# Kernel optimization log

Measured on AMD Instinct MI355X. Metric: run time of the kernel, lower is better.

## Reference

```python
import jax, jax.numpy as jnp
import numpy as np

N_HEAD = 16


def setup_inputs() -> dict:
    key = jax.random.key(0)
    k1, k2, k3 = jax.random.split(key, 3)
    B, T, C = 4, 2048, 1024
    x = jax.random.normal(k1, (B, T, C), dtype=jnp.float32)
    Wqkv = jax.random.normal(k2, (C, 3 * C), dtype=jnp.float32) * 0.02
    Wproj = jax.random.normal(k3, (C, C), dtype=jnp.float32) * 0.02
    return {"x": x, "Wqkv": Wqkv, "Wproj": Wproj}


def reference(x, Wqkv, Wproj):
    B, T, C = x.shape
    nh = N_HEAD
    hd = C // nh
    qkv = x @ Wqkv                                  # (B, T, 3C)
    q, k, v = jnp.split(qkv, 3, axis=-1)
    # (B, T, C) -> (B, nh, T, hd)
    q = q.reshape(B, T, nh, hd).transpose(0, 2, 1, 3)
    k = k.reshape(B, T, nh, hd).transpose(0, 2, 1, 3)
    v = v.reshape(B, T, nh, hd).transpose(0, 2, 1, 3)
    # scaled dot-product attention with causal mask (past_kv=None => T_all == T)
    att = jnp.einsum("bhtd,bhsd->bhts", q, k) / jnp.sqrt(jnp.float32(hd))
    causal = jnp.tril(jnp.ones((T, T), dtype=bool))  # (T, T)
    att = jnp.where(causal[None, None, :, :], att, jnp.float32(-jnp.inf))
    att = jax.nn.softmax(att, axis=-1)              # (B, nh, T, T)
    y = jnp.einsum("bhts,bhsd->bhtd", att, v)       # (B, nh, T, hd)
    y = y.transpose(0, 2, 1, 3).reshape(B, T, C)
    y = y @ Wproj                                   # (B, T, C)
    # present_kv (detached in original)
    return y, jax.lax.stop_gradient(k), jax.lax.stop_gradient(v)
```

## Files before the change

kernel.cpp:

```cpp
#include <hip/hip_runtime.h>
#include <hip/hip_bf16.h>


typedef __bf16 bf16;
typedef __attribute__((ext_vector_type(8))) __bf16 bf16x8;
typedef __attribute__((ext_vector_type(4))) __bf16 bf16x4;
typedef __attribute__((ext_vector_type(4))) float f32x4;

#define AS_G __attribute__((address_space(1)))
#define AS_L __attribute__((address_space(3)))

#define QSCALE 0.1803368801111204f

__device__ __forceinline__ void gld_lds16(const bf16* g, bf16* l) {
  __builtin_amdgcn_global_load_lds((const AS_G void*)g, (AS_L void*)l, 16, 0, 0);
}

__global__ __launch_bounds__(256) void k_cast(const float* __restrict__ in,
                                              bf16* __restrict__ out, int n) {
  int i = (blockIdx.x * 256 + threadIdx.x) * 8;
  if (i >= n) return;
  float4 a = *(const float4*)(in + i);
  float4 b = *(const float4*)(in + i + 4);
  bf16x8 o;
  o[0] = (bf16)a.x; o[1] = (bf16)a.y; o[2] = (bf16)a.z; o[3] = (bf16)a.w;
  o[4] = (bf16)b.x; o[5] = (bf16)b.y; o[6] = (bf16)b.z; o[7] = (bf16)b.w;
  *(bf16x8*)(out + i) = o;
}

__global__ __launch_bounds__(256) void k_transpose(const float* __restrict__ in,
                                                   bf16* __restrict__ out,
                                                   int K, int N) {
  __shared__ float tile[32][33];
  int bx = blockIdx.x * 32;
  int by = blockIdx.y * 32;
  int tx = threadIdx.x, ty = threadIdx.y;
#pragma unroll
  for (int i = 0; i < 4; ++i)
    tile[ty + i * 8][tx] = in[(size_t)(by + ty + i * 8) * N + bx + tx];
  __syncthreads();
#pragma unroll
  for (int i = 0; i < 4; ++i)
    out[(size_t)(bx + ty + i * 8) * K + by + tx] = (bf16)tile[tx][ty + i * 8];
}

__device__ __forceinline__ void gemm_main_256x128(const bf16* __restrict__ A,
                                                  const bf16* __restrict__ Bt,
                                                  int m0, int n0,
                                                  bf16* As, bf16* Bs,
                                                  f32x4 acc[4][4]) {
  const int tid = threadIdx.x;
  const int w = tid >> 6, lane = tid & 63, lo = lane & 15, hi = lane >> 4;
  const int wm = w >> 1, wn = w & 1;
  const int urow = tid >> 3;
  const int gsw = (tid & 7) ^ (urow & 7);
  const bf16* ga = A + (size_t)(m0 + urow) * 1024 + gsw * 8;
  const bf16* gb = Bt + (size_t)(n0 + urow) * 1024 + gsw * 8;
  const int p0 = hi ^ (lo & 7);
  const int aRow = wm * 64 + lo;
  const int bRow = wn * 64 + lo;

#define STAGE_A2(t, bufi, s0) do {                                                              \
    gld_lds16(ga + (size_t)(s0) * 65536 + (t) * 64,                                             \
              As + (bufi) * 16384 + (s0) * 4096 + w * 512);                                     \
    gld_lds16(ga + (size_t)((s0) + 1) * 65536 + (t) * 64,                                       \
              As + (bufi) * 16384 + ((s0) + 1) * 4096 + w * 512);                               \
  } while (0)
#define STAGE_B2(t, bufi) do {                                                                  \
    gld_lds16(gb + (t) * 64, Bs + (bufi) * 8192 + w * 512);                                     \
    gld_lds16(gb + 65536 + (t) * 64, Bs + (bufi) * 8192 + 4096 + w * 512);                      \
  } while (0)

  STAGE_A2(0, 0, 0); STAGE_A2(0, 0, 2); STAGE_B2(0, 0);
  STAGE_A2(1, 1, 0); STAGE_A2(1, 1, 2); STAGE_B2(1, 1);

  bf16x8 a[2][2], b[4][2];
  int buf = 0, sbuf = 2;
#pragma unroll 1
  for (int t = 0; t < 16; ++t) {
    if (t < 15) asm volatile("s_waitcnt vmcnt(6)" ::: "memory");
    else        asm volatile("s_waitcnt vmcnt(0)" ::: "memory");
    __builtin_amdgcn_s_barrier();
    const bf16* Ab = As + buf * 16384;
    const bf16* Bb = Bs + buf * 8192;

#pragma unroll
    for (int mi = 0; mi < 2; ++mi) {
      const bf16* r = Ab + (aRow + mi * 16) * 64;
      a[mi][0] = *(const bf16x8*)(r + p0 * 8);
      a[mi][1] = *(const bf16x8*)(r + (p0 ^ 4) * 8);
    }
#pragma unroll
    for (int ni = 0; ni < 2; ++ni) {
      const bf16* r = Bb + (bRow + ni * 16) * 64;
      b[ni][0] = *(const bf16x8*)(r + p0 * 8);
      b[ni][1] = *(const bf16x8*)(r + (p0 ^ 4) * 8);
    }
    if (t < 14) STAGE_A2(t + 2, sbuf, 0);
    __builtin_amdgcn_s_barrier();
    __builtin_amdgcn_s_setprio(1);
#pragma unroll
    for (int ks = 0; ks < 2; ++ks)
#pragma unroll
      for (int mi = 0; mi < 2; ++mi)
#pragma unroll
        for (int ni = 0; ni < 2; ++ni)
          acc[mi][ni] = __builtin_amdgcn_mfma_f32_16x16x32_bf16(a[mi][ks], b[ni][ks], acc[mi][ni], 0, 0, 0);
    __builtin_amdgcn_s_setprio(0);
    __builtin_amdgcn_s_barrier();

#pragma unroll
    for (int ni = 0; ni < 2; ++ni) {
      const bf16* r = Bb + (bRow + (ni + 2) * 16) * 64;
      b[ni + 2][0] = *(const bf16x8*)(r + p0 * 8);
      b[ni + 2][1] = *(const bf16x8*)(r + (p0 ^ 4) * 8);
    }
    if (t < 14) STAGE_A2(t + 2, sbuf, 2);
    __builtin_amdgcn_s_barrier();
    __builtin_amdgcn_s_setprio(1);
#pragma unroll
    for (int ks = 0; ks < 2; ++ks)
#pragma unroll
      for (int mi = 0; mi < 2; ++mi)
#pragma unroll
        for (int ni = 0; ni < 2; ++ni)
          acc[mi][ni + 2] = __builtin_amdgcn_mfma_f32_16x16x32_bf16(a[mi][ks], b[ni + 2][ks], acc[mi][ni + 2], 0, 0, 0);
    __builtin_amdgcn_s_setprio(0);
    __builtin_amdgcn_s_barrier();

#pragma unroll
    for (int mi = 0; mi < 2; ++mi) {
      const bf16* r = Ab + (aRow + (mi + 2) * 16) * 64;
      a[mi][0] = *(const bf16x8*)(r + p0 * 8);
      a[mi][1] = *(const bf16x8*)(r + (p0 ^ 4) * 8);
    }
    if (t < 14) STAGE_B2(t + 2, sbuf);
    __builtin_amdgcn_s_barrier();
    __builtin_amdgcn_s_setprio(1);
#pragma unroll
    for (int ks = 0; ks < 2; ++ks)
#pragma unroll
      for (int mi = 0; mi < 2; ++mi)
#pragma unroll
        for (int ni = 0; ni < 2; ++ni)
          acc[mi + 2][ni + 2] = __builtin_amdgcn_mfma_f32_16x16x32_bf16(a[mi][ks], b[ni + 2][ks], acc[mi + 2][ni + 2], 0, 0, 0);
    __builtin_amdgcn_s_setprio(0);
    __builtin_amdgcn_s_barrier();

    __builtin_amdgcn_s_setprio(1);
#pragma unroll
    for (int ks = 0; ks < 2; ++ks)
#pragma unroll
      for (int mi = 0; mi < 2; ++mi)
#pragma unroll
        for (int ni = 0; ni < 2; ++ni)
          acc[mi + 2][ni] = __builtin_amdgcn_mfma_f32_16x16x32_bf16(a[mi][ks], b[ni][ks], acc[mi + 2][ni], 0, 0, 0);
    __builtin_amdgcn_s_setprio(0);

    buf = (buf == 2) ? 0 : buf + 1;
    sbuf = (sbuf == 2) ? 0 : sbuf + 1;
  }
#undef STAGE_A2
#undef STAGE_B2
}

__global__ __launch_bounds__(512, 2) void k_gemm_qkv(const bf16* __restrict__ x,
                                                     const bf16* __restrict__ WqkvT,
                                                     bf16* __restrict__ qb, bf16* __restrict__ kb,
                                                     bf16* __restrict__ vtb,
                                                     float* __restrict__ outk, float* __restrict__ outv) {
  __shared__ bf16 As[49152], Bs[24576];
  int id = blockIdx.x;
  int swz = (id & 7) * 96 + (id >> 3);
  int by = swz / 24, bx = swz - by * 24;
  int m0 = by * 256, n0 = bx * 128;
  f32x4 acc[4][4] = {};
  gemm_main_256x128(x, WqkvT, m0, n0, As, Bs, acc);
  const int tid = threadIdx.x;
  const int w = tid >> 6, lane = tid & 63, lo = lane & 15, hi = lane >> 4;
  const int wm = w >> 1, wn = w & 1;
#pragma unroll
  for (int mi = 0; mi < 4; ++mi) {
    int growbase = m0 + wm * 64 + mi * 16 + hi * 4;
    int bb = growbase >> 11, t0 = growbase & 2047;
#pragma unroll
    for (int ni = 0; ni < 4; ++ni) {
      int gcol = n0 + wn * 64 + ni * 16 + lo;
      int part = gcol >> 10;
      int cc = gcol & 1023, h = cc >> 6, d = cc & 63;
      size_t idx0 = ((size_t)(bb * 16 + h) * 2048 + t0) * 64 + d;
      if (part == 0) {
#pragma unroll
        for (int r = 0; r < 4; ++r) qb[idx0 + (size_t)r * 64] = (bf16)(acc[mi][ni][r] * QSCALE);
      } else if (part == 1) {
#pragma unroll
        for (int r = 0; r < 4; ++r) {
          float val = acc[mi][ni][r];
          kb[idx0 + (size_t)r * 64] = (bf16)val;
          outk[idx0 + (size_t)r * 64] = val;
        }
      } else {
        bf16x4 pk;
#pragma unroll
        for (int r = 0; r < 4; ++r) {
          float val = acc[mi][ni][r];
          outv[idx0 + (size_t)r * 64] = val;
          pk[r] = (bf16)val;
        }
        *(bf16x4*)(vtb + ((size_t)(bb * 16 + h) * 64 + d) * 2048 + t0) = pk;
      }
    }
  }
}

__global__ __launch_bounds__(512, 2) void k_gemm_proj(const bf16* __restrict__ yb,
                                                      const bf16* __restrict__ WprojT,
                                                      float* __restrict__ out) {
  __shared__ bf16 As[49152], Bs[24576];
  int id = blockIdx.x;
  int swz = (id & 7) * 32 + (id >> 3);
  int by = swz >> 3, bx = swz & 7;
  int m0 = by * 256, n0 = bx * 128;
  f32x4 acc[4][4] = {};
  gemm_main_256x128(yb, WprojT, m0, n0, As, Bs, acc);
  const int tid = threadIdx.x;
  const int w = tid >> 6, lane = tid & 63, lo = lane & 15, hi = lane >> 4;
  const int wm = w >> 1, wn = w & 1;
#pragma unroll
  for (int mi = 0; mi < 4; ++mi)
#pragma unroll
    for (int ni = 0; ni < 4; ++ni)
#pragma unroll
      for (int r = 0; r < 4; ++r) {
        int grow = m0 + wm * 64 + mi * 16 + hi * 4 + r;
        int gcol = n0 + wn * 64 + ni * 16 + lo;
        out[(size_t)grow * 1024 + gcol] = acc[mi][ni][r];
      }
}

__device__ __forceinline__ void p_store(f32x4 sacc[4], bool mask,
                                        int w, int lo, int hi, bf16* psrow) {
  if (mask) {
#pragma unroll
    for (int nt = 0; nt < 4; ++nt)
#pragma unroll
      for (int r = 0; r < 4; ++r)
        if (nt * 16 + hi * 4 + r > w * 16 + lo) sacc[nt][r] = -1e30f;
  }
#pragma unroll
  for (int nt = 0; nt < 4; ++nt) {
    bf16x4 pk;
#pragma unroll
    for (int r = 0; r < 4; ++r) pk[r] = (bf16)exp2f(sacc[nt][r]);
    *(bf16x4*)(psrow + (w * 16 + lo) * 72 + nt * 16 + hi * 4) = pk;
  }
}

__device__ __forceinline__ void write_y(bf16* __restrict__ y, int b, int h, int qrow,
                                        int hi, const f32x4 o[4], float inv) {
  size_t base = ((size_t)b * 2048 + qrow) * 1024 + h * 64;
#pragma unroll
  for (int mt = 0; mt < 4; ++mt) {
    bf16x4 yk;
#pragma unroll
    for (int r = 0; r < 4; ++r) yk[r] = (bf16)(o[mt][r] * inv);
    *(bf16x4*)(y + base + mt * 16 + hi * 4) = yk;
  }
}

__global__ __launch_bounds__(256, 4) void k_flash(const bf16* __restrict__ q,
                                                  const bf16* __restrict__ k,
                                                  const bf16* __restrict__ vt,
                                                  bf16* __restrict__ y) {
  __shared__ bf16 Ks[64 * 64];
  __shared__ bf16 Vs[80 * 64];
  __shared__ bf16 Ps[128 * 72];
  const int bi = blockIdx.x;
  const int slot = bi >> 3;
  const int bh = (bi & 7) + 8 * (slot >> 4);
  const int j = slot & 15;
  const int jA = j, jB = 31 - j;
  const int tid = threadIdx.x, w = tid >> 6, lane = tid & 63, lo = lane & 15, hi = lane >> 4;
  const bf16* qp = q + (size_t)bh * 2048 * 64;
  const bf16* kp = k + (size_t)bh * 2048 * 64;
  const bf16* vtp = vt + (size_t)bh * 64 * 2048;

  {
    int rr = tid >> 4, c = (tid & 15) * 4;
    bf16x4 z;
    bf16 v1 = (rr == 0) ? (bf16)1.0f : (bf16)0.0f;
    z[0] = v1; z[1] = v1; z[2] = v1; z[3] = v1;
    *(bf16x4*)(Vs + (64 + rr) * 64 + c) = z;
  }

  bf16x8 qfA[2], qfB[2];
  {
    int qA = jA * 64 + w * 16 + lo;
    int qB = jB * 64 + w * 16 + lo;
    qfA[0] = *(const bf16x8*)(qp + (size_t)qA * 64 + hi * 8);
    qfA[1] = *(const bf16x8*)(qp + (size_t)qA * 64 + 32 + hi * 8);
    qfB[0] = *(const bf16x8*)(qp + (size_t)qB * 64 + hi * 8);
    qfB[1] = *(const bf16x8*)(qp + (size_t)qB * 64 + 32 + hi * 8);
  }
  f32x4 oA[4] = {}, oB[4] = {};
  f32x4 oLA = {}, oLB = {};

  for (int st = 0; st <= jB; ++st) {
    const int s0 = st * 64;
#pragma unroll
    for (int p = 0; p < 2; ++p) {
      int u = tid + 256 * p;
      int row = u >> 3, c = u & 7, g = c ^ (row & 7);
      gld_lds16(kp + (size_t)(s0 + row) * 64 + g * 8, Ks + p * 2048 + w * 512);
      gld_lds16(vtp + (size_t)row * 2048 + s0 + g * 8, Vs + p * 2048 + w * 512);
    }
    __syncthreads();

    bf16x8 kf[4][2];
#pragma unroll
    for (int nt = 0; nt < 4; ++nt)
#pragma unroll
      for (int ks = 0; ks < 2; ++ks)
        kf[nt][ks] = *(const bf16x8*)(Ks + (nt * 16 + lo) * 64 + ((ks * 4 + hi) ^ (lo & 7)) * 8);

    const bool actA = (st <= jA);
    if (actA) {
      f32x4 sacc[4] = {};
#pragma unroll
      for (int nt = 0; nt < 4; ++nt)
#pragma unroll
        for (int ks = 0; ks < 2; ++ks)
          sacc[nt] = __builtin_amdgcn_mfma_f32_16x16x32_bf16(kf[nt][ks], qfA[ks], sacc[nt], 0, 0, 0);
      p_store(sacc, st == jA, w, lo, hi, Ps);
    }
    {
      f32x4 sacc[4] = {};
#pragma unroll
      for (int nt = 0; nt < 4; ++nt)
#pragma unroll
        for (int ks = 0; ks < 2; ++ks)
          sacc[nt] = __builtin_amdgcn_mfma_f32_16x16x32_bf16(kf[nt][ks], qfB[ks], sacc[nt], 0, 0, 0);
      p_store(sacc, st == jB, w, lo, hi, Ps + 64 * 72);
    }
    __asm__ volatile("s_waitcnt lgkmcnt(0)" ::: "memory");

    bf16x8 pfA[2], pfB[2];
#pragma unroll
    for (int ks = 0; ks < 2; ++ks) {
      pfB[ks] = *(const bf16x8*)(Ps + (64 + w * 16 + lo) * 72 + ks * 32 + hi * 8);
      if (actA) pfA[ks] = *(const bf16x8*)(Ps + (w * 16 + lo) * 72 + ks * 32 + hi * 8);
    }
#pragma unroll
    for (int mt = 0; mt < 5; ++mt) {
#pragma unroll
      for (int ks = 0; ks < 2; ++ks) {
        int row = mt * 16 + lo;
        bf16x8 vf = *(const bf16x8*)(Vs + row * 64 + ((ks * 4 + hi) ^ (row & 7)) * 8);
        if (mt < 4) {
          oB[mt] = __builtin_amdgcn_mfma_f32_16x16x32_bf16(vf, pfB[ks], oB[mt], 0, 0, 0);
          if (actA) oA[mt] = __builtin_amdgcn_mfma_f32_16x16x32_bf16(vf, pfA[ks], oA[mt], 0, 0, 0);
        } else {
          oLB = __builtin_amdgcn_mfma_f32_16x16x32_bf16(vf, pfB[ks], oLB, 0, 0, 0);
          if (actA) oLA = __builtin_amdgcn_mfma_f32_16x16x32_bf16(vf, pfA[ks], oLA, 0, 0, 0);
        }
      }
    }
    __syncthreads();
  }

  const int b = bh >> 4, h = bh & 15;
  float lA = __shfl(oLA[0], lo, 64);
  float lB = __shfl(oLB[0], lo, 64);
  write_y(y, b, h, jA * 64 + w * 16 + lo, hi, oA, 1.0f / lA);
  write_y(y, b, h, jB * 64 + w * 16 + lo, hi, oB, 1.0f / lB);
}

extern "C" void kernel_launch(void* const* d_in, const int* in_sizes, int n_in,
                              void* d_out, int out_size, void* d_ws, size_t ws_size,
                              hipStream_t stream) {
  const float* x = (const float*)d_in[0];
  const float* Wqkv = (const float*)d_in[1];
  const float* Wproj = (const float*)d_in[2];
  float* out = (float*)d_out;

  const size_t YSZ = (size_t)8192 * 1024;
  char* ws = (char*)d_ws;
  bf16* xb = (bf16*)ws;      ws += (size_t)8192 * 1024 * 2;
  bf16* wqkvT = (bf16*)ws;   ws += (size_t)3072 * 1024 * 2;
  bf16* wprojT = (bf16*)ws;  ws += (size_t)1024 * 1024 * 2;
  bf16* qb = (bf16*)ws;      ws += (size_t)64 * 2048 * 64 * 2;
  bf16* kb = (bf16*)ws;      ws += (size_t)64 * 2048 * 64 * 2;
  bf16* vtb = (bf16*)ws;     ws += (size_t)64 * 2048 * 64 * 2;
  bf16* yb = (bf16*)ws;

  float* outy = out;
  float* outk = out + YSZ;
  float* outv = out + 2 * YSZ;

  k_cast<<<4096, 256, 0, stream>>>(x, xb, 8388608);
  dim3 tb(32, 8);
  k_transpose<<<dim3(96, 32), tb, 0, stream>>>(Wqkv, wqkvT, 1024, 3072);
  k_transpose<<<dim3(32, 32), tb, 0, stream>>>(Wproj, wprojT, 1024, 1024);
  k_gemm_qkv<<<768, 512, 0, stream>>>(xb, wqkvT, qb, kb, vtb, outk, outv);
  k_flash<<<1024, 256, 0, stream>>>(qb, kb, vtb, yb);
  k_gemm_proj<<<256, 512, 0, stream>>>(yb, wprojT, outy);
}
```

Measured before the change: 309.0 us.

## Double-buffer K/V in flash kernel and merge prep kernels into one launch

The flash attention kernel now double-buffers K and V tiles in LDS, prefetching the next tile while computing the current one, and waits on vmcnt before a barrier instead of using a synchronous load-then-sync loop. The ones-row used for the row-sum trick moves to its own LDS buffer, the P stride changes to 76 to reduce bank conflicts, raw exp2 is used, and s_setprio is raised around MFMA blocks. The cast and two transpose kernels are merged into a single launch to cut launch overhead. The extra LDS reduces the room for multiple blocks per CU, which may cost occupancy.

```diff
diff --git a/kernel.cpp b/kernel.cpp
--- a/kernel.cpp
+++ b/kernel.cpp
@@ -16,32 +16,34 @@
   __builtin_amdgcn_global_load_lds((const AS_G void*)g, (AS_L void*)l, 16, 0, 0);
 }
 
-__global__ __launch_bounds__(256) void k_cast(const float* __restrict__ in,
-                                              bf16* __restrict__ out, int n) {
-  int i = (blockIdx.x * 256 + threadIdx.x) * 8;
-  if (i >= n) return;
-  float4 a = *(const float4*)(in + i);
-  float4 b = *(const float4*)(in + i + 4);
-  bf16x8 o;
-  o[0] = (bf16)a.x; o[1] = (bf16)a.y; o[2] = (bf16)a.z; o[3] = (bf16)a.w;
-  o[4] = (bf16)b.x; o[5] = (bf16)b.y; o[6] = (bf16)b.z; o[7] = (bf16)b.w;
-  *(bf16x8*)(out + i) = o;
-}
-
-__global__ __launch_bounds__(256) void k_transpose(const float* __restrict__ in,
-                                                   bf16* __restrict__ out,
-                                                   int K, int N) {
+__global__ __launch_bounds__(256) void k_prep(const float* __restrict__ x, bf16* __restrict__ xb,
+                                              const float* __restrict__ Wqkv, bf16* __restrict__ wqkvT,
+                                              const float* __restrict__ Wproj, bf16* __restrict__ wprojT) {
   __shared__ float tile[32][33];
-  int bx = blockIdx.x * 32;
-  int by = blockIdx.y * 32;
-  int tx = threadIdx.x, ty = threadIdx.y;
+  const int bid = blockIdx.x, tid = threadIdx.x;
+  if (bid < 4096) {
+    int i = (bid * 256 + tid) * 8;
+    float4 a = *(const float4*)(x + i);
+    float4 b = *(const float4*)(x + i + 4);
+    bf16x8 o;
+    o[0] = (bf16)a.x; o[1] = (bf16)a.y; o[2] = (bf16)a.z; o[3] = (bf16)a.w;
+    o[4] = (bf16)b.x; o[5] = (bf16)b.y; o[6] = (bf16)b.z; o[7] = (bf16)b.w;
+    *(bf16x8*)(xb + i) = o;
+    return;
+  }
+  const float* in; bf16* out; int N, t;
+  if (bid < 7168) { t = bid - 4096; N = 3072; in = Wqkv; out = wqkvT; }
+  else            { t = bid - 7168; N = 1024; in = Wproj; out = wprojT; }
+  const int nbx = N >> 5;
+  const int bx = (t % nbx) * 32, by = (t / nbx) * 32;
+  const int tx = tid & 31, ty = tid >> 5;
 #pragma unroll
   for (int i = 0; i < 4; ++i)
     tile[ty + i * 8][tx] = in[(size_t)(by + ty + i * 8) * N + bx + tx];
   __syncthreads();
 #pragma unroll
   for (int i = 0; i < 4; ++i)
-    out[(size_t)(bx + ty + i * 8) * K + by + tx] = (bf16)tile[tx][ty + i * 8];
+    out[(size_t)(bx + ty + i * 8) * 1024 + by + tx] = (bf16)tile[tx][ty + i * 8];
 }
 
 __device__ __forceinline__ void gemm_main_256x128(const bf16* __restrict__ A,
@@ -238,6 +240,8 @@
       }
 }
 
+#define PSTR 76
+
 __device__ __forceinline__ void p_store(f32x4 sacc[4], bool mask,
                                         int w, int lo, int hi, bf16* psrow) {
   if (mask) {
@@ -251,8 +255,8 @@
   for (int nt = 0; nt < 4; ++nt) {
     bf16x4 pk;
 #pragma unroll
-    for (int r = 0; r < 4; ++r) pk[r] = (bf16)exp2f(sacc[nt][r]);
-    *(bf16x4*)(psrow + (w * 16 + lo) * 72 + nt * 16 + hi * 4) = pk;
+    for (int r = 0; r < 4; ++r) pk[r] = (bf16)__builtin_amdgcn_exp2f(sacc[nt][r]);
+    *(bf16x4*)(psrow + (w * 16 + lo) * PSTR + nt * 16 + hi * 4) = pk;
   }
 }
 
@@ -272,9 +276,10 @@
                                                   const bf16* __restrict__ k,
                                                   const bf16* __restrict__ vt,
                                                   bf16* __restrict__ y) {
-  __shared__ bf16 Ks[64 * 64];
-  __shared__ bf16 Vs[80 * 64];
-  __shared__ bf16 Ps[128 * 72];
+  __shared__ bf16 Ks[2 * 4096];
+  __shared__ bf16 Vs[2 * 4096];
+  __shared__ bf16 Ones[16 * 64];
+  __shared__ bf16 Ps[128 * PSTR];
   const int bi = blockIdx.x;
   const int slot = bi >> 3;
   const int bh = (bi & 7) + 8 * (slot >> 4);
@@ -290,7 +295,15 @@
     bf16x4 z;
     bf16 v1 = (rr == 0) ? (bf16)1.0f : (bf16)0.0f;
     z[0] = v1; z[1] = v1; z[2] = v1; z[3] = v1;
-    *(bf16x4*)(Vs + (64 + rr) * 64 + c) = z;
+    *(bf16x4*)(Ones + rr * 64 + c) = z;
+  }
+
+#pragma unroll
+  for (int p = 0; p < 2; ++p) {
+    int u = tid + 256 * p;
+    int row = u >> 3, g = (u & 7) ^ (row & 7);
+    gld_lds16(kp + (size_t)row * 64 + g * 8, Ks + p * 2048 + w * 512);
+    gld_lds16(vtp + (size_t)row * 2048 + g * 8, Vs + p * 2048 + w * 512);
   }
 
   bf16x8 qfA[2], qfB[2];
@@ -305,57 +318,66 @@
   f32x4 oA[4] = {}, oB[4] = {};
   f32x4 oLA = {}, oLB = {};
 
+  asm volatile("s_waitcnt vmcnt(0)" ::: "memory");
+  __builtin_amdgcn_s_barrier();
+
   for (int st = 0; st <= jB; ++st) {
-    const int s0 = st * 64;
-#pragma unroll
-    for (int p = 0; p < 2; ++p) {
-      int u = tid + 256 * p;
-      int row = u >> 3, c = u & 7, g = c ^ (row & 7);
-      gld_lds16(kp + (size_t)(s0 + row) * 64 + g * 8, Ks + p * 2048 + w * 512);
-      gld_lds16(vtp + (size_t)row * 2048 + s0 + g * 8, Vs + p * 2048 + w * 512);
-    }
-    __syncthreads();
+    const int cb = (st & 1) * 4096;
+    const int nb = cb ^ 4096;
 
     bf16x8 kf[4][2];
 #pragma unroll
     for (int nt = 0; nt < 4; ++nt)
 #pragma unroll
       for (int ks = 0; ks < 2; ++ks)
-        kf[nt][ks] = *(const bf16x8*)(Ks + (nt * 16 + lo) * 64 + ((ks * 4 + hi) ^ (lo & 7)) * 8);
+        kf[nt][ks] = *(const bf16x8*)(Ks + cb + (nt * 16 + lo) * 64 + ((ks * 4 + hi) ^ (lo & 7)) * 8);
+
+    if (st < jB) {
+      const int s1 = (st + 1) * 64;
+#pragma unroll
+      for (int p = 0; p < 2; ++p) {
+        int u = tid + 256 * p;
+        int row = u >> 3, g = (u & 7) ^ (row & 7);
+        gld_lds16(kp + (size_t)(s1 + row) * 64 + g * 8, Ks + nb + p * 2048 + w * 512);
+        gld_lds16(vtp + (size_t)row * 2048 + s1 + g * 8, Vs + nb + p * 2048 + w * 512);
+      }
+    }
 
     const bool actA = (st <= jA);
+    f32x4 saccA[4] = {}, saccB[4] = {};
+    __builtin_amdgcn_s_setprio(1);
     if (actA) {
-      f32x4 sacc[4] = {};
 #pragma unroll
       for (int nt = 0; nt < 4; ++nt)
 #pragma unroll
         for (int ks = 0; ks < 2; ++ks)
-          sacc[nt] = __builtin_amdgcn_mfma_f32_16x16x32_bf16(kf[nt][ks], qfA[ks], sacc[nt], 0, 0, 0);
-      p_store(sacc, st == jA, w, lo, hi, Ps);
-    }
-    {
-      f32x4 sacc[4] = {};
-#pragma unroll
-      for (int nt = 0; nt < 4; ++nt)
-#pragma unroll
-        for (int ks = 0; ks < 2; ++ks)
-          sacc[nt] = __builtin_amdgcn_mfma_f32_16x16x32_bf16(kf[nt][ks], qfB[ks], sacc[nt], 0, 0, 0);
-      p_store(sacc, st == jB, w, lo, hi, Ps + 64 * 72);
-    }
+          saccA[nt] = __builtin_amdgcn_mfma_f32_16x16x32_bf16(kf[nt][ks], qfA[ks], saccA[nt], 0, 0, 0);
+    }
+#pragma unroll
+    for (int nt = 0; nt < 4; ++nt)
+#pragma unroll
+      for (int ks = 0; ks < 2; ++ks)
+        saccB[nt] = __builtin_amdgcn_mfma_f32_16x16x32_bf16(kf[nt][ks], qfB[ks], saccB[nt], 0, 0, 0);
+    __builtin_amdgcn_s_setprio(0);
+    if (actA) p_store(saccA, st == jA, w, lo, hi, Ps);
+    p_store(saccB, st == jB, w, lo, hi, Ps + 64 * PSTR);
     __asm__ volatile("s_waitcnt lgkmcnt(0)" ::: "memory");
 
     bf16x8 pfA[2], pfB[2];
 #pragma unroll
     for (int ks = 0; ks < 2; ++ks) {
-      pfB[ks] = *(const bf16x8*)(Ps + (64 + w * 16 + lo) * 72 + ks * 32 + hi * 8);
-      if (actA) pfA[ks] = *(const bf16x8*)(Ps + (w * 16 + lo) * 72 + ks * 32 + hi * 8);
-    }
+      pfB[ks] = *(const bf16x8*)(Ps + (64 + w * 16 + lo) * PSTR + ks * 32 + hi * 8);
+      if (actA) pfA[ks] = *(const bf16x8*)(Ps + (w * 16 + lo) * PSTR + ks * 32 + hi * 8);
+    }
+    __builtin_amdgcn_s_setprio(1);
 #pragma unroll
     for (int mt = 0; mt < 5; ++mt) {
 #pragma unroll
       for (int ks = 0; ks < 2; ++ks) {
         int row = mt * 16 + lo;
-        bf16x8 vf = *(const bf16x8*)(Vs + row * 64 + ((ks * 4 + hi) ^ (row & 7)) * 8);
+        bf16x8 vf = (mt < 4)
+            ? *(const bf16x8*)(Vs + cb + row * 64 + ((ks * 4 + hi) ^ (row & 7)) * 8)
+            : *(const bf16x8*)(Ones + lo * 64 + ((ks * 4 + hi) ^ (lo & 7)) * 8);
         if (mt < 4) {
           oB[mt] = __builtin_amdgcn_mfma_f32_16x16x32_bf16(vf, pfB[ks], oB[mt], 0, 0, 0);
           if (actA) oA[mt] = __builtin_amdgcn_mfma_f32_16x16x32_bf16(vf, pfA[ks], oA[mt], 0, 0, 0);
@@ -365,7 +387,10 @@
         }
       }
     }
-    __syncthreads();
+    __builtin_amdgcn_s_setprio(0);
+
+    asm volatile("s_waitcnt vmcnt(0)" ::: "memory");
+    __builtin_amdgcn_s_barrier();
   }
 
   const int b = bh >> 4, h = bh & 15;
@@ -397,10 +422,7 @@
   float* outk = out + YSZ;
   float* outv = out + 2 * YSZ;
 
-  k_cast<<<4096, 256, 0, stream>>>(x, xb, 8388608);
-  dim3 tb(32, 8);
-  k_transpose<<<dim3(96, 32), tb, 0, stream>>>(Wqkv, wqkvT, 1024, 3072);
-  k_transpose<<<dim3(32, 32), tb, 0, stream>>>(Wproj, wprojT, 1024, 1024);
+  k_prep<<<8192, 256, 0, stream>>>(x, xb, Wqkv, wqkvT, Wproj, wprojT);
   k_gemm_qkv<<<768, 512, 0, stream>>>(xb, wqkvT, qb, kb, vtb, outk, outv);
   k_flash<<<1024, 256, 0, stream>>>(qb, kb, vtb, yb);
   k_gemm_proj<<<256, 512, 0, stream>>>(yb, wprojT, outy);
```

Result: faster. 301.0 us (-2.6%).
